# Kernel optimization log

Measured on AMD Instinct MI355X. Metric: run time of the kernel, lower is better.

Reference implementation:

```python
import jax, jax.numpy as jnp
import numpy as np

N = 100000  # nodes
E = 1600000  # edges (before self-loops)
F_IN, F_HID, F_OUT = 64, 128, 64


def setup_inputs() -> dict:
    key = jax.random.key(0)
    ks = jax.random.split(key, 8)
    x = jax.random.normal(ks[0], (N, F_IN), dtype=jnp.float32)
    edge_index = jax.random.randint(ks[1], (2, E), 0, N, dtype=jnp.int64)
    # Glorot-ish init for weights, zero bias (PyG GCNConv default)
    W1 = jax.random.normal(ks[2], (F_IN, F_HID), dtype=jnp.float32) / np.sqrt(F_IN)
    W2 = jax.random.normal(ks[3], (F_HID, F_HID), dtype=jnp.float32) / np.sqrt(F_HID)
    W3 = jax.random.normal(ks[4], (F_HID, F_OUT), dtype=jnp.float32) / np.sqrt(F_HID)
    b1 = jnp.zeros((F_HID,), dtype=jnp.float32)
    b2 = jnp.zeros((F_HID,), dtype=jnp.float32)
    b3 = jnp.zeros((F_OUT,), dtype=jnp.float32)
    return {"x": x, "edge_index": edge_index, "W1": W1, "b1": b1,
            "W2": W2, "b2": b2, "W3": W3, "b3": b3}


def _gcn_norm(edge_index, num_nodes):
    """Add self-loops and compute symmetric D^-1/2 A D^-1/2 edge norms."""
    loop = jnp.arange(num_nodes, dtype=edge_index.dtype)
    src = jnp.concatenate([edge_index[0], loop])  # [E+N]
    dst = jnp.concatenate([edge_index[1], loop])  # [E+N]
    deg = jax.ops.segment_sum(jnp.ones_like(src, dtype=jnp.float32), dst,
                              num_segments=num_nodes)
    dinv = jnp.where(deg > 0, jax.lax.rsqrt(deg), 0.0)
    norm = dinv[src] * dinv[dst]  # [E+N]
    return src, dst, norm


def _gcn_conv(h, src, dst, norm, W, b, num_nodes):
    hw = h @ W                                   # [N, out] dense transform
    msg = hw[src] * norm[:, None]                # gather + edge scale
    out = jax.ops.segment_sum(msg, dst, num_segments=num_nodes)  # scatter-add
    return out + b


def reference(x, edge_index, W1, b1, W2, b2, W3, b3):
    src, dst, norm = _gcn_norm(edge_index, N)
    h = jax.nn.relu(_gcn_conv(x, src, dst, norm, W1, b1, N))
    h = jax.nn.relu(_gcn_conv(h, src, dst, norm, W2, b2, N))
    return _gcn_conv(h, src, dst, norm, W3, b3, N)
```

## Files before the change

kernel.cpp:

```cpp
#include <hip/hip_runtime.h>
#include <hip/hip_bf16.h>
#include <hip/hip_fp16.h>


typedef _Float16 h8 __attribute__((ext_vector_type(8)));
typedef float f4 __attribute__((ext_vector_type(4)));

constexpr int BSHIFT = 7;
constexpr int BNODES = 1 << BSHIFT;
constexpr int PB     = 256;
constexpr int CAP    = 4096;

__device__ inline void load8h(const _Float16* p, float* f) {
    h8 v = *(const h8*)p;
#pragma unroll
    for (int j = 0; j < 8; j++) f[j] = (float)v[j];
}

__device__ inline void store8h(_Float16* p, const float* f) {
    h8 v;
#pragma unroll
    for (int j = 0; j < 8; j++) v[j] = (_Float16)f[j];
    *(h8*)p = v;
}

__device__ inline void store4h(_Float16* p, float4 v) {
    _Float16 t[4] = {(_Float16)v.x, (_Float16)v.y, (_Float16)v.z, (_Float16)v.w};
    *(uint2*)p = *(uint2*)t;
}

__global__ __launch_bounds__(256) void phist_k(const int* __restrict__ dst,
                                               int* __restrict__ hist,
                                               int E, int nbuck, int chunk) {
    __shared__ int h[1024];
    for (int i = threadIdx.x; i < nbuck; i += 256) h[i] = 0;
    __syncthreads();
    int beg = blockIdx.x * chunk;
    int end = min(E, beg + chunk);
    for (int e = beg + threadIdx.x; e < end; e += 256)
        atomicAdd(&h[dst[e] >> BSHIFT], 1);
    __syncthreads();
    for (int i = threadIdx.x; i < nbuck; i += 256)
        hist[(long)blockIdx.x * nbuck + i] = h[i];
}

__global__ __launch_bounds__(256) void scan_blocks_k(const int* __restrict__ in,
                                                     int* __restrict__ excl,
                                                     int* __restrict__ bsums, int n) {
    __shared__ int s[256];
    int tid = threadIdx.x;
    int i = blockIdx.x * 256 + tid;
    int v = (i < n) ? in[i] : 0;
    s[tid] = v;
    __syncthreads();
    for (int off = 1; off < 256; off <<= 1) {
        int t = (tid >= off) ? s[tid - off] : 0;
        __syncthreads();
        s[tid] += t;
        __syncthreads();
    }
    if (i < n) excl[i] = s[tid] - v;
    if (tid == 255) bsums[blockIdx.x] = s[255];
}

__global__ __launch_bounds__(1024) void mid_k(int* __restrict__ bsums, int nb,
                                              const int* __restrict__ hist,
                                              int* __restrict__ bbase,
                                              int nbuck, int E) {
    __shared__ int s[1024];
    int tid = threadIdx.x;
    int v = 0;
    if (blockIdx.x == 0) {
        v = (tid < nb) ? bsums[tid] : 0;
    } else {
        if (tid < nbuck) {
            int t0 = 0, t1 = 0, t2 = 0, t3 = 0;
            for (int j = 0; j < PB; j += 4) {
                t0 += hist[(long)(j + 0) * nbuck + tid];
                t1 += hist[(long)(j + 1) * nbuck + tid];
                t2 += hist[(long)(j + 2) * nbuck + tid];
                t3 += hist[(long)(j + 3) * nbuck + tid];
            }
            v = (t0 + t1) + (t2 + t3);
        }
    }
    s[tid] = v;
    __syncthreads();
    for (int off = 1; off < 1024; off <<= 1) {
        int t = (tid >= off) ? s[tid - off] : 0;
        __syncthreads();
        s[tid] += t;
        __syncthreads();
    }
    if (blockIdx.x == 0) {
        if (tid < nb) bsums[tid] = s[tid] - v;
    } else {
        if (tid < nbuck) bbase[tid] = s[tid] - v;
        if (tid == 0) bbase[nbuck] = E;
    }
}

__global__ __launch_bounds__(256) void part2_k(const int* __restrict__ src,
                                               const int* __restrict__ dst,
                                               const int* __restrict__ offs,
                                               const int* __restrict__ bsums,
                                               unsigned* __restrict__ ebuf,
                                               int E, int nbuck, int chunk) {
    __shared__ int cur[1024];
    for (int i = threadIdx.x; i < nbuck; i += 256) {
        long flat = (long)blockIdx.x * nbuck + i;
        cur[i] = offs[flat] + bsums[flat >> 8];
    }
    __syncthreads();
    int beg = blockIdx.x * chunk;
    int end = min(E, beg + chunk);
    for (int e = beg + threadIdx.x; e < end; e += 256) {
        int d = dst[e];
        int b = d >> BSHIFT;
        int pos = atomicAdd(&cur[b], 1);
        ebuf[pos] = ((unsigned)(d & (BNODES - 1)) << 25) | (unsigned)src[e];
    }
}

__global__ __launch_bounds__(256) void finalize_k(const unsigned* __restrict__ ebuf,
                                                  const int* __restrict__ hist,
                                                  const int* __restrict__ offs,
                                                  const int* __restrict__ bsums,
                                                  const int* __restrict__ bbase,
                                                  int nbuck,
                                                  int* __restrict__ rowst,
                                                  int* __restrict__ rowend,
                                                  float* __restrict__ dinv,
                                                  int* __restrict__ col,
                                                  const float* __restrict__ x,
                                                  _Float16* __restrict__ msgX, int N) {
    __shared__ unsigned se[CAP];
    __shared__ int cj[PB], sj[PB], sb[PB];
    __shared__ int cnt_s[BNODES], scan_s[BNODES], cur_s[BNODES];
    __shared__ float di_s[BNODES];

    int b = blockIdx.x, tid = threadIdx.x;
    int node0 = b << BSHIFT;
    int nn = min(BNODES, N - node0);
    int beg = bbase[b];

    if (tid < PB) {
        long flat = (long)tid * nbuck + b;
        cj[tid] = hist[flat];
        sj[tid] = offs[flat] + bsums[flat >> 8];
    }
    if (tid < BNODES) cnt_s[tid] = 0;
    __syncthreads();

    if (tid < PB) sb[tid] = cj[tid];
    __syncthreads();
    for (int off = 1; off < PB; off <<= 1) {
        int t = 0;
        if (tid < PB && tid >= off) t = sb[tid - off];
        __syncthreads();
        if (tid < PB) sb[tid] += t;
        __syncthreads();
    }
    int m = sb[PB - 1];
    __syncthreads();

    {
        int j = tid;
        int base = sb[j] - cj[j], c = cj[j], s0 = sj[j];
        for (int k = 0; k < c; k++) {
            unsigned e = ebuf[s0 + k];
            int idx = base + k;
            if (idx < CAP) se[idx] = e;
            else atomicAdd(&cnt_s[e >> 25], 1);
        }
    }
    __syncthreads();

    int mcap = m < CAP ? m : CAP;
    for (int i = tid; i < mcap; i += 256) atomicAdd(&cnt_s[se[i] >> 25], 1);
    __syncthreads();

    int v = (tid < BNODES) ? cnt_s[tid] : 0;
    if (tid < BNODES) scan_s[tid] = v;
    __syncthreads();
    for (int off = 1; off < BNODES; off <<= 1) {
        int t = 0;
        if (tid < BNODES && tid >= off) t = scan_s[tid - off];
        __syncthreads();
        if (tid < BNODES) scan_s[tid] += t;
        __syncthreads();
    }
    if (tid < nn) {
        int ex = scan_s[tid] - v;
        int st = beg + ex;
        rowst[node0 + tid] = st;
        rowend[node0 + tid] = st + v;
        float di = rsqrtf((float)v + 1.0f);
        dinv[node0 + tid] = di;
        di_s[tid] = di;
        cur_s[tid] = ex;
    }
    __syncthreads();

    for (int i = tid; i < mcap; i += 256) {
        unsigned e = se[i];
        int p = atomicAdd(&cur_s[e >> 25], 1);
        col[beg + p] = (int)(e & 0x1FFFFFFu);
    }
    if (m > CAP) {
        int j = tid;
        int base = sb[j] - cj[j], c = cj[j], s0 = sj[j];
        for (int k = 0; k < c; k++) {
            int idx = base + k;
            if (idx >= CAP) {
                unsigned e = ebuf[s0 + k];
                int p = atomicAdd(&cur_s[e >> 25], 1);
                col[beg + p] = (int)(e & 0x1FFFFFFu);
            }
        }
    }

    for (int t = tid; t < nn * 16; t += 256) {
        int nl = t >> 4, q = t & 15;
        int node = node0 + nl;
        float4 vx = *(const float4*)(x + (long)node * 64 + q * 4);
        float di = di_s[nl];
        vx.x *= di; vx.y *= di; vx.z *= di; vx.w *= di;
        store4h(msgX + (long)node * 64 + q * 4, vx);
    }
}

template <int K, int FOUT, bool BIAS, bool RELU, bool DINV_OUT, bool SMOUT>
__global__ __launch_bounds__(256) void fag_k(const _Float16* __restrict__ msg,
                                             const int* __restrict__ rowst,
                                             const int* __restrict__ rowend,
                                             const int* __restrict__ col,
                                             const float* __restrict__ dinv,
                                             const _Float16* __restrict__ Wsw,
                                             const float* __restrict__ bias,
                                             _Float16* __restrict__ C, int n) {
    constexpr int NT = FOUT / 16, NC = K / 32;
    constexpr int LDK = K + 8;
    constexpr int LPN = K / 8;
    constexpr int NPB = 256 / LPN;
    constexpr int CC = 2560;
    __shared__ _Float16 As[64 * LDK];
    __shared__ int cls[CC];

    int tid = threadIdx.x;
    int row0 = blockIdx.x * 64;

    int lastn = min(row0 + 64, n) - 1;
    int beg0 = rowst[row0];
    int win  = rowend[lastn] - beg0;
    int wl = min(win, CC);
    for (int i = tid; i < wl; i += 256) cls[i] = col[beg0 + i];
    __syncthreads();
    const int* cb = (win <= CC) ? (const int*)cls : (col + beg0);

#pragma unroll
    for (int pass = 0; pass < 64 / NPB; pass++) {
        int nl = pass * NPB + tid / LPN;
        int q = tid % LPN;
        int node = row0 + nl;
        float acc[8];
        if (node < n) {
            load8h(msg + (long)node * K + q * 8, acc);
            int beg = rowst[node] - beg0, end = rowend[node] - beg0;
            int e = beg;
            for (; e + 4 <= end; e += 4) {
                int s0 = cb[e], s1 = cb[e + 1], s2 = cb[e + 2], s3 = cb[e + 3];
                h8 v0 = *(const h8*)(msg + (long)s0 * K + q * 8);
                h8 v1 = *(const h8*)(msg + (long)s1 * K + q * 8);
                h8 v2 = *(const h8*)(msg + (long)s2 * K + q * 8);
                h8 v3 = *(const h8*)(msg + (long)s3 * K + q * 8);
#pragma unroll
                for (int j = 0; j < 8; j++)
                    acc[j] += ((float)v0[j] + (float)v1[j]) + ((float)v2[j] + (float)v3[j]);
            }
            for (; e < end; e++) {
                int s = cb[e];
                h8 v = *(const h8*)(msg + (long)s * K + q * 8);
#pragma unroll
                for (int j = 0; j < 8; j++) acc[j] += (float)v[j];
            }
            float di = dinv[node];
#pragma unroll
            for (int j = 0; j < 8; j++) acc[j] *= di;
        } else {
#pragma unroll
            for (int j = 0; j < 8; j++) acc[j] = 0.f;
        }
        h8 o;
#pragma unroll
        for (int j = 0; j < 8; j++) o[j] = (_Float16)acc[j];
        *(h8*)(As + nl * LDK + q * 8) = o;
    }
    __syncthreads();

    int lane = tid & 63, wave = tid >> 6;
    int quad = lane >> 4, cl = lane & 15;
    int r0 = wave * 16;

    h8 a[NC];
#pragma unroll
    for (int c = 0; c < NC; c++)
        a[c] = *(const h8*)(As + (r0 + cl) * LDK + quad * 8 + c * 32);

    f4 acc2[NT];
#pragma unroll
    for (int t = 0; t < NT; t++) acc2[t] = (f4){0.f, 0.f, 0.f, 0.f};

    const h8* wv = (const h8*)Wsw;
#pragma unroll
    for (int c = 0; c < NC; c++) {
#pragma unroll
        for (int t = 0; t < NT; t++)
            acc2[t] = __builtin_amdgcn_mfma_f32_16x16x32_f16(
                a[c], wv[(c * NT + t) * 64 + lane], acc2[t], 0, 0, 0);
    }

#pragma unroll
    for (int t = 0; t < NT; t++) {
        int c0 = t * 16 + cl;
        float bb = BIAS ? bias[c0] : 0.f;
#pragma unroll
        for (int r = 0; r < 4; r++) {
            int row = row0 + r0 + quad * 4 + r;
            if (row >= n) continue;
            float v = acc2[t][r] + bb;
            if (RELU) v = fmaxf(v, 0.f);
            if (DINV_OUT) v *= dinv[row];
            if (SMOUT)
                C[((long)t * n + row) * 16 + cl] = (_Float16)v;
            else
                C[(long)row * FOUT + c0] = (_Float16)v;
        }
    }
}

__global__ __launch_bounds__(256) void agg_ep2_k(const _Float16* __restrict__ msg,
                                                 const int* __restrict__ rowst,
                                                 const int* __restrict__ rowend,
                                                 const int* __restrict__ col,
                                                 const float* __restrict__ dinv,
                                                 _Float16* __restrict__ out, int n) {
    constexpr int CC = 1536;
    __shared__ int cls[CC];
    int slice = blockIdx.x & 7;
    int blk   = blockIdx.x >> 3;
    int tid   = threadIdx.x;
    int node0b = blk * 32;

    int lastn = min(node0b + 32, n) - 1;
    int beg0 = rowst[node0b];
    int win  = rowend[lastn] - beg0;
    int wl = min(win, CC);
    for (int i = tid; i < wl; i += 256) cls[i] = col[beg0 + i];
    __syncthreads();
    const int* cb = (win <= CC) ? (const int*)cls : (col + beg0);

    int node  = node0b + (tid >> 3);
    int eslot = (tid >> 1) & 3;
    int q     = tid & 1;
    if (node >= n) return;
    const _Float16* mp = msg + (long)slice * n * 16 + q * 8;

    float acc[8];
    if (eslot == 0) {
        load8h(mp + (long)node * 16, acc);
    } else {
#pragma unroll
        for (int j = 0; j < 8; j++) acc[j] = 0.f;
    }

    int beg = rowst[node] - beg0, end = rowend[node] - beg0;
    int e = beg + eslot;
    for (; e + 12 < end; e += 16) {
        int s0 = cb[e], s1 = cb[e + 4], s2 = cb[e + 8], s3 = cb[e + 12];
        h8 v0 = *(const h8*)(mp + (long)s0 * 16);
        h8 v1 = *(const h8*)(mp + (long)s1 * 16);
        h8 v2 = *(const h8*)(mp + (long)s2 * 16);
        h8 v3 = *(const h8*)(mp + (long)s3 * 16);
#pragma unroll
        for (int j = 0; j < 8; j++)
            acc[j] += (((float)v0[j] + (float)v1[j]) + ((float)v2[j] + (float)v3[j]));
    }
    for (; e < end; e += 4) {
        int s = cb[e];
        h8 v = *(const h8*)(mp + (long)s * 16);
#pragma unroll
        for (int j = 0; j < 8; j++) acc[j] += (float)v[j];
    }

#pragma unroll
    for (int j = 0; j < 8; j++) {
        acc[j] += __shfl_xor(acc[j], 2);
        acc[j] += __shfl_xor(acc[j], 4);
    }

    if ((tid & 6) == 0) {
        float di = dinv[node];
        float o[8];
#pragma unroll
        for (int j = 0; j < 8; j++) o[j] = di * acc[j];
        store8h(out + ((long)slice * n + node) * 16 + q * 8, o);
    }
}

template <int F, bool BIAS, bool F16OUT>
__global__ __launch_bounds__(256) void agg_f16_k(const _Float16* __restrict__ msg,
                                                 const int* __restrict__ rowst,
                                                 const int* __restrict__ rowend,
                                                 const int* __restrict__ col,
                                                 const float* __restrict__ dinv,
                                                 const float* __restrict__ b,
                                                 void* __restrict__ out, int n) {
    constexpr int LPN = F / 8;
    constexpr int NPB = 256 / LPN;
    constexpr int CC = NPB * 48;
    __shared__ int cls[CC];
    int tid = threadIdx.x;
    int node0b = blockIdx.x * NPB;

    int lastn = min(node0b + NPB, n) - 1;
    int beg0 = rowst[node0b];
    int win  = rowend[lastn] - beg0;
    int wl = min(win, CC);
    for (int i = tid; i < wl; i += 256) cls[i] = col[beg0 + i];
    __syncthreads();
    const int* cb = (win <= CC) ? (const int*)cls : (col + beg0);

    int node = node0b + tid / LPN;
    int q = tid % LPN;
    if (node >= n) return;

    float acc[8];
    load8h(msg + (long)node * F + q * 8, acc);

    int beg = rowst[node] - beg0, end = rowend[node] - beg0;
    int e = beg;
    for (; e + 8 <= end; e += 8) {
        h8 v[8];
#pragma unroll
        for (int u = 0; u < 8; u++)
            v[u] = *(const h8*)(msg + (long)cb[e + u] * F + q * 8);
#pragma unroll
        for (int j = 0; j < 8; j++)
            acc[j] += (((float)v[0][j] + (float)v[1][j]) + ((float)v[2][j] + (float)v[3][j])) +
                      (((float)v[4][j] + (float)v[5][j]) + ((float)v[6][j] + (float)v[7][j]));
    }
    for (; e + 4 <= end; e += 4) {
        h8 v0 = *(const h8*)(msg + (long)cb[e] * F + q * 8);
        h8 v1 = *(const h8*)(msg + (long)cb[e + 1] * F + q * 8);
        h8 v2 = *(const h8*)(msg + (long)cb[e + 2] * F + q * 8);
        h8 v3 = *(const h8*)(msg + (long)cb[e + 3] * F + q * 8);
#pragma unroll
        for (int j = 0; j < 8; j++)
            acc[j] += ((float)v0[j] + (float)v1[j]) + ((float)v2[j] + (float)v3[j]);
    }
    for (; e < end; e++) {
        h8 v = *(const h8*)(msg + (long)cb[e] * F + q * 8);
#pragma unroll
        for (int j = 0; j < 8; j++) acc[j] += (float)v[j];
    }

    float di = dinv[node];
    float o[8];
#pragma unroll
    for (int j = 0; j < 8; j++) o[j] = di * acc[j];
    if (BIAS) {
#pragma unroll
        for (int j = 0; j < 8; j++) o[j] += b[q * 8 + j];
    }
    if (F16OUT) {
        store8h((_Float16*)out + (long)node * F + q * 8, o);
    } else {
        float* dst = (float*)out + (long)node * F + q * 8;
        *(float4*)dst = make_float4(o[0], o[1], o[2], o[3]);
        *(float4*)(dst + 4) = make_float4(o[4], o[5], o[6], o[7]);
    }
}

template <int K, int FOUT>
__device__ inline void wfrag(const float* __restrict__ W,
                             _Float16* __restrict__ Wsw, int t) {
    constexpr int NT = FOUT / 16;
    int lane = t & 63;
    int tile = (t >> 6) % NT;
    int chunk = (t >> 6) / NT;
    int kbase = chunk * 32 + (lane >> 4) * 8;
    int nc = tile * 16 + (lane & 15);
    h8 v;
#pragma unroll
    for (int j = 0; j < 8; j++) v[j] = (_Float16)W[(kbase + j) * FOUT + nc];
    ((h8*)Wsw)[t] = v;
}

__global__ __launch_bounds__(256) void wprep3_k(const float* __restrict__ W1,
                                                const float* __restrict__ W2,
                                                const float* __restrict__ W3,
                                                _Float16* __restrict__ w1s,
                                                _Float16* __restrict__ w2s,
                                                _Float16* __restrict__ w3s) {
    int t = blockIdx.x * 256 + threadIdx.x;
    if (t < 1024) wfrag<64, 128>(W1, w1s, t);
    else if (t < 3072) wfrag<128, 128>(W2, w2s, t - 1024);
    else if (t < 4096) wfrag<128, 64>(W3, w3s, t - 3072);
}

__global__ __launch_bounds__(256) void dgemm_k(const _Float16* __restrict__ A,
                                               const _Float16* __restrict__ w2s,
                                               const _Float16* __restrict__ w3s,
                                               const float* __restrict__ b2,
                                               const float* __restrict__ dinv,
                                               _Float16* __restrict__ C, int n) {
    constexpr int LDK = 136;
    __shared__ _Float16 Hs[64 * LDK];

    int tid = threadIdx.x, lane = tid & 63, wave = tid >> 6;
    int quad = lane >> 4, cl = lane & 15;
    int row0 = blockIdx.x * 64, r0 = wave * 16;
    int arow = row0 + r0 + cl;

    h8 a[4];
#pragma unroll
    for (int c = 0; c < 4; c++) {
        int sl = c * 2 + (quad >> 1);
        a[c] = *(const h8*)(A + ((long)sl * n + arow) * 16 + (quad & 1) * 8);
    }

    f4 acc1[8];
#pragma unroll
    for (int t = 0; t < 8; t++) acc1[t] = (f4){0.f, 0.f, 0.f, 0.f};
    const h8* wv2 = (const h8*)w2s;
#pragma unroll
    for (int c = 0; c < 4; c++) {
#pragma unroll
        for (int t = 0; t < 8; t++)
            acc1[t] = __builtin_amdgcn_mfma_f32_16x16x32_f16(
                a[c], wv2[(c * 8 + t) * 64 + lane], acc1[t], 0, 0, 0);
    }

#pragma unroll
    for (int t = 0; t < 8; t++) {
        int c0 = t * 16 + cl;
        float bb = b2[c0];
#pragma unroll
        for (int r = 0; r < 4; r++) {
            float v = fmaxf(acc1[t][r] + bb, 0.f);
            Hs[(r0 + quad * 4 + r) * LDK + c0] = (_Float16)v;
        }
    }
    __builtin_amdgcn_s_waitcnt(0);

    h8 a2[4];
#pragma unroll
    for (int c = 0; c < 4; c++)
        a2[c] = *(const h8*)(Hs + (r0 + cl) * LDK + quad * 8 + c * 32);

    f4 acc2[4];
#pragma unroll
    for (int t = 0; t < 4; t++) acc2[t] = (f4){0.f, 0.f, 0.f, 0.f};
    const h8* wv3 = (const h8*)w3s;
#pragma unroll
    for (int c = 0; c < 4; c++) {
#pragma unroll
        for (int t = 0; t < 4; t++)
            acc2[t] = __builtin_amdgcn_mfma_f32_16x16x32_f16(
                a2[c], wv3[(c * 4 + t) * 64 + lane], acc2[t], 0, 0, 0);
    }

#pragma unroll
    for (int t = 0; t < 4; t++) {
        int c0 = t * 16 + cl;
#pragma unroll
        for (int r = 0; r < 4; r++) {
            int row = row0 + r0 + quad * 4 + r;
            if (row >= n) continue;
            float v = acc2[t][r] * dinv[row];
            C[(long)row * 64 + c0] = (_Float16)v;
        }
    }
}

extern "C" void kernel_launch(void* const* d_in, const int* in_sizes, int n_in,
                              void* d_out, int out_size, void* d_ws, size_t ws_size,
                              hipStream_t stream) {
    const float* x  = (const float*)d_in[0];
    const int*   ei = (const int*)d_in[1];
    const float* W1 = (const float*)d_in[2];
    const float* b1 = (const float*)d_in[3];
    const float* W2 = (const float*)d_in[4];
    const float* b2 = (const float*)d_in[5];
    const float* W3 = (const float*)d_in[6];
    const float* b3 = (const float*)d_in[7];
    float* out = (float*)d_out;

    const int N = in_sizes[0] / 64;
    const int E = in_sizes[1] / 2;
    const int* src = ei;
    const int* dst = ei + E;
    const int nbuck = (N + BNODES - 1) >> BSHIFT;
    const int chunk = (E + PB - 1) / PB;
    const int n2 = PB * nbuck;
    const int nb2 = (n2 + 255) / 256;

    int*   hist   = (int*)d_ws;
    int*   offs   = hist + n2;
    int*   bsums  = offs + n2;
    int*   bbase  = bsums + 1024;
    int*   rowst  = bbase + nbuck + 1;
    int*   rowend = rowst + N;
    float* dinv   = (float*)(rowend + N);
    int*   col    = (int*)(dinv + N);
    _Float16* w1s = (_Float16*)(col + E);
    _Float16* w2s = w1s + 64 * 128;
    _Float16* w3s = w2s + 128 * 128;
    float* P      = (float*)(w3s + 128 * 64);
    float* Q      = P + (long)N * 128;

    _Float16* msgX  = (_Float16*)P;
    unsigned* ebuf  = (unsigned*)Q;
    _Float16* msg1  = (_Float16*)Q;
    _Float16* aggH2 = (_Float16*)P;
    _Float16* msg3  = (_Float16*)Q;

    const int gb = (N + 63) / 64;

    wprep3_k<<<16, 256, 0, stream>>>(W1, W2, W3, w1s, w2s, w3s);

    phist_k<<<PB, 256, 0, stream>>>(dst, hist, E, nbuck, chunk);
    scan_blocks_k<<<nb2, 256, 0, stream>>>(hist, offs, bsums, n2);
    mid_k<<<2, 1024, 0, stream>>>(bsums, nb2, hist, bbase, nbuck, E);
    part2_k<<<PB, 256, 0, stream>>>(src, dst, offs, bsums, ebuf, E, nbuck, chunk);
    finalize_k<<<nbuck, 256, 0, stream>>>(ebuf, hist, offs, bsums, bbase, nbuck,
                                          rowst, rowend, dinv, col, x, msgX, N);

    fag_k<64, 128, true, true, true, true><<<gb, 256, 0, stream>>>(
        msgX, rowst, rowend, col, dinv, w1s, b1, msg1, N);

    const int nb32 = (N + 31) / 32;
    agg_ep2_k<<<8 * nb32, 256, 0, stream>>>(
        msg1, rowst, rowend, col, dinv, aggH2, N);

    dgemm_k<<<gb, 256, 0, stream>>>(aggH2, w2s, w3s, b2, dinv, msg3, N);

    agg_f16_k<64, true, false><<<(N + 31) / 32, 256, 0, stream>>>(
        msg3, rowst, rowend, col, dinv, b3, (void*)out, N);
}
```

Measured before the change: 375.5 us.

## Split layer-2 aggregation by source-node half to localize gathers

Finalize now partitions each node's CSR row into edges whose source lies in the lower or upper half of node IDs and records a midpoint. The layer-2 aggregation runs as 4 feature slices of 32 halves times 2 source halves, so each block gathers from a smaller region of the message array, which is meant to improve cache hit rate. The two partial sums plus the self message are combined and scaled by dinv in the dgemm prologue. This costs an extra partial buffer write and read and more atomics in finalize.

```diff
diff --git a/kernel.cpp b/kernel.cpp
--- a/kernel.cpp
+++ b/kernel.cpp
@@ -130,13 +130,16 @@
                                                   int nbuck,
                                                   int* __restrict__ rowst,
                                                   int* __restrict__ rowend,
+                                                  int* __restrict__ midp,
                                                   float* __restrict__ dinv,
                                                   int* __restrict__ col,
                                                   const float* __restrict__ x,
-                                                  _Float16* __restrict__ msgX, int N) {
+                                                  _Float16* __restrict__ msgX,
+                                                  int N, int H) {
     __shared__ unsigned se[CAP];
     __shared__ int cj[PB], sj[PB], sb[PB];
-    __shared__ int cnt_s[BNODES], scan_s[BNODES], cur_s[BNODES];
+    __shared__ int cnt_s[BNODES], cntA_s[BNODES], scan_s[BNODES];
+    __shared__ int cur_s[BNODES], curB_s[BNODES];
     __shared__ float di_s[BNODES];
 
     int b = blockIdx.x, tid = threadIdx.x;
@@ -149,7 +152,7 @@
         cj[tid] = hist[flat];
         sj[tid] = offs[flat] + bsums[flat >> 8];
     }
-    if (tid < BNODES) cnt_s[tid] = 0;
+    if (tid < BNODES) { cnt_s[tid] = 0; cntA_s[tid] = 0; }
     __syncthreads();
 
     if (tid < PB) sb[tid] = cj[tid];
@@ -171,13 +174,20 @@
             unsigned e = ebuf[s0 + k];
             int idx = base + k;
             if (idx < CAP) se[idx] = e;
-            else atomicAdd(&cnt_s[e >> 25], 1);
+            else {
+                atomicAdd(&cnt_s[e >> 25], 1);
+                if ((int)(e & 0x1FFFFFFu) < H) atomicAdd(&cntA_s[e >> 25], 1);
+            }
         }
     }
     __syncthreads();
 
     int mcap = m < CAP ? m : CAP;
-    for (int i = tid; i < mcap; i += 256) atomicAdd(&cnt_s[se[i] >> 25], 1);
+    for (int i = tid; i < mcap; i += 256) {
+        unsigned e = se[i];
+        atomicAdd(&cnt_s[e >> 25], 1);
+        if ((int)(e & 0x1FFFFFFu) < H) atomicAdd(&cntA_s[e >> 25], 1);
+    }
     __syncthreads();
 
     int v = (tid < BNODES) ? cnt_s[tid] : 0;
@@ -193,19 +203,23 @@
     if (tid < nn) {
         int ex = scan_s[tid] - v;
         int st = beg + ex;
+        int ca = cntA_s[tid];
         rowst[node0 + tid] = st;
         rowend[node0 + tid] = st + v;
+        midp[node0 + tid] = st + ca;
         float di = rsqrtf((float)v + 1.0f);
         dinv[node0 + tid] = di;
         di_s[tid] = di;
         cur_s[tid] = ex;
+        curB_s[tid] = ex + ca;
     }
     __syncthreads();
 
     for (int i = tid; i < mcap; i += 256) {
         unsigned e = se[i];
-        int p = atomicAdd(&cur_s[e >> 25], 1);
-        col[beg + p] = (int)(e & 0x1FFFFFFu);
+        int s = (int)(e & 0x1FFFFFFu), d = e >> 25;
+        int p = (s < H) ? atomicAdd(&cur_s[d], 1) : atomicAdd(&curB_s[d], 1);
+        col[beg + p] = s;
     }
     if (m > CAP) {
         int j = tid;
@@ -214,8 +228,9 @@
             int idx = base + k;
             if (idx >= CAP) {
                 unsigned e = ebuf[s0 + k];
-                int p = atomicAdd(&cur_s[e >> 25], 1);
-                col[beg + p] = (int)(e & 0x1FFFFFFu);
+                int s = (int)(e & 0x1FFFFFFu), d = e >> 25;
+                int p = (s < H) ? atomicAdd(&cur_s[d], 1) : atomicAdd(&curB_s[d], 1);
+                col[beg + p] = s;
             }
         }
     }
@@ -332,22 +347,23 @@
             if (RELU) v = fmaxf(v, 0.f);
             if (DINV_OUT) v *= dinv[row];
             if (SMOUT)
-                C[((long)t * n + row) * 16 + cl] = (_Float16)v;
+                C[((long)(t >> 1) * n + row) * 32 + (t & 1) * 16 + cl] = (_Float16)v;
             else
                 C[(long)row * FOUT + c0] = (_Float16)v;
         }
     }
 }
 
-__global__ __launch_bounds__(256) void agg_ep2_k(const _Float16* __restrict__ msg,
-                                                 const int* __restrict__ rowst,
-                                                 const int* __restrict__ rowend,
-                                                 const int* __restrict__ col,
-                                                 const float* __restrict__ dinv,
-                                                 _Float16* __restrict__ out, int n) {
+__global__ __launch_bounds__(256) void agg_h2_k(const _Float16* __restrict__ msg,
+                                                const int* __restrict__ rowst,
+                                                const int* __restrict__ midp,
+                                                const int* __restrict__ rowend,
+                                                const int* __restrict__ col,
+                                                _Float16* __restrict__ part, int n) {
     constexpr int CC = 1536;
     __shared__ int cls[CC];
-    int slice = blockIdx.x & 7;
+    int idx7  = blockIdx.x & 7;
+    int slice = idx7 & 3, half = idx7 >> 2;
     int blk   = blockIdx.x >> 3;
     int tid   = threadIdx.x;
     int node0b = blk * 32;
@@ -361,50 +377,40 @@
     const int* cb = (win <= CC) ? (const int*)cls : (col + beg0);
 
     int node  = node0b + (tid >> 3);
-    int eslot = (tid >> 1) & 3;
-    int q     = tid & 1;
+    int eslot = (tid >> 2) & 1;
+    int q     = tid & 3;
     if (node >= n) return;
-    const _Float16* mp = msg + (long)slice * n * 16 + q * 8;
+    const _Float16* mp = msg + (long)slice * n * 32 + q * 8;
 
     float acc[8];
-    if (eslot == 0) {
-        load8h(mp + (long)node * 16, acc);
-    } else {
-#pragma unroll
-        for (int j = 0; j < 8; j++) acc[j] = 0.f;
-    }
-
-    int beg = rowst[node] - beg0, end = rowend[node] - beg0;
+#pragma unroll
+    for (int j = 0; j < 8; j++) acc[j] = 0.f;
+
+    int beg = (half ? midp[node] : rowst[node]) - beg0;
+    int end = (half ? rowend[node] : midp[node]) - beg0;
     int e = beg + eslot;
-    for (; e + 12 < end; e += 16) {
-        int s0 = cb[e], s1 = cb[e + 4], s2 = cb[e + 8], s3 = cb[e + 12];
-        h8 v0 = *(const h8*)(mp + (long)s0 * 16);
-        h8 v1 = *(const h8*)(mp + (long)s1 * 16);
-        h8 v2 = *(const h8*)(mp + (long)s2 * 16);
-        h8 v3 = *(const h8*)(mp + (long)s3 * 16);
+    for (; e + 6 < end; e += 8) {
+        int s0 = cb[e], s1 = cb[e + 2], s2 = cb[e + 4], s3 = cb[e + 6];
+        h8 v0 = *(const h8*)(mp + (long)s0 * 32);
+        h8 v1 = *(const h8*)(mp + (long)s1 * 32);
+        h8 v2 = *(const h8*)(mp + (long)s2 * 32);
+        h8 v3 = *(const h8*)(mp + (long)s3 * 32);
 #pragma unroll
         for (int j = 0; j < 8; j++)
             acc[j] += (((float)v0[j] + (float)v1[j]) + ((float)v2[j] + (float)v3[j]));
     }
-    for (; e < end; e += 4) {
+    for (; e < end; e += 2) {
         int s = cb[e];
-        h8 v = *(const h8*)(mp + (long)s * 16);
+        h8 v = *(const h8*)(mp + (long)s * 32);
 #pragma unroll
         for (int j = 0; j < 8; j++) acc[j] += (float)v[j];
     }
 
 #pragma unroll
-    for (int j = 0; j < 8; j++) {
-        acc[j] += __shfl_xor(acc[j], 2);
-        acc[j] += __shfl_xor(acc[j], 4);
-    }
-
-    if ((tid & 6) == 0) {
-        float di = dinv[node];
-        float o[8];
-#pragma unroll
-        for (int j = 0; j < 8; j++) o[j] = di * acc[j];
-        store8h(out + ((long)slice * n + node) * 16 + q * 8, o);
+    for (int j = 0; j < 8; j++) acc[j] += __shfl_xor(acc[j], 4);
+
+    if (eslot == 0) {
+        store8h(part + (((long)half * 4 + slice) * n + node) * 32 + q * 8, acc);
     }
 }
 
@@ -509,7 +515,8 @@
     else if (t < 4096) wfrag<128, 64>(W3, w3s, t - 3072);
 }
 
-__global__ __launch_bounds__(256) void dgemm_k(const _Float16* __restrict__ A,
+__global__ __launch_bounds__(256) void dgemm_k(const _Float16* __restrict__ part,
+                                               const _Float16* __restrict__ selfm,
                                                const _Float16* __restrict__ w2s,
                                                const _Float16* __restrict__ w3s,
                                                const float* __restrict__ b2,
@@ -523,11 +530,24 @@
     int row0 = blockIdx.x * 64, r0 = wave * 16;
     int arow = row0 + r0 + cl;
 
+    const _Float16* pA = part;
+    const _Float16* pB = part + (long)4 * n * 32;
+    float di = dinv[arow];
+
     h8 a[4];
 #pragma unroll
     for (int c = 0; c < 4; c++) {
-        int sl = c * 2 + (quad >> 1);
-        a[c] = *(const h8*)(A + ((long)sl * n + arow) * 16 + (quad & 1) * 8);
+        long off = ((long)c * n + arow) * 32 + quad * 8;
+        h8 va = *(const h8*)(pA + off);
+        h8 vb = *(const h8*)(pB + off);
+        h8 vs = *(const h8*)(selfm + off);
+        h8 o;
+#pragma unroll
+        for (int j = 0; j < 8; j++) {
+            float f = (((float)va[j] + (float)vb[j]) + (float)vs[j]) * di;
+            o[j] = (_Float16)f;
+        }
+        a[c] = o;
     }
 
     f4 acc1[8];
@@ -621,10 +641,11 @@
     float* Q      = P + (long)N * 128;
 
     _Float16* msgX  = (_Float16*)P;
+    _Float16* part  = (_Float16*)P;
     unsigned* ebuf  = (unsigned*)Q;
     _Float16* msg1  = (_Float16*)Q;
-    _Float16* aggH2 = (_Float16*)P;
-    _Float16* msg3  = (_Float16*)Q;
+    _Float16* msg3  = (_Float16*)(Q + (long)N * 64);
+    int*      midp  = (int*)(Q + (long)N * 96);
 
     const int gb = (N + 63) / 64;
 
@@ -635,16 +656,17 @@
     mid_k<<<2, 1024, 0, stream>>>(bsums, nb2, hist, bbase, nbuck, E);
     part2_k<<<PB, 256, 0, stream>>>(src, dst, offs, bsums, ebuf, E, nbuck, chunk);
     finalize_k<<<nbuck, 256, 0, stream>>>(ebuf, hist, offs, bsums, bbase, nbuck,
-                                          rowst, rowend, dinv, col, x, msgX, N);
+                                          rowst, rowend, midp, dinv, col, x,
+                                          msgX, N, N / 2);
 
     fag_k<64, 128, true, true, true, true><<<gb, 256, 0, stream>>>(
         msgX, rowst, rowend, col, dinv, w1s, b1, msg1, N);
 
     const int nb32 = (N + 31) / 32;
-    agg_ep2_k<<<8 * nb32, 256, 0, stream>>>(
-        msg1, rowst, rowend, col, dinv, aggH2, N);
-
-    dgemm_k<<<gb, 256, 0, stream>>>(aggH2, w2s, w3s, b2, dinv, msg3, N);
+    agg_h2_k<<<8 * nb32, 256, 0, stream>>>(
+        msg1, rowst, midp, rowend, col, part, N);
+
+    dgemm_k<<<gb, 256, 0, stream>>>(part, msg1, w2s, w3s, b2, dinv, msg3, N);
 
     agg_f16_k<64, true, false><<<(N + 31) / 32, 256, 0, stream>>>(
         msg3, rowst, rowend, col, dinv, b3, (void*)out, N);
```

Result: faster. 364.0 us (-3.1%).
